# Optimization experiments

Measured on AMD Instinct MI355X. Metric: run time of the kernel, lower is better.

## Reference

```python
import jax, jax.numpy as jnp
import numpy as np

EPS = 1e-6


def _ring_view(t, start, length, M):
    # contiguous logical view of `length` oldest positions starting at start
    if start + length <= M:
        return t[:, start:start + length]
    first = t[:, start:]
    return jnp.concatenate([first, t[:, :length - first.shape[1]]], axis=1)


def _ring_write(t, start, chunk, M):
    # write chunk at logical position `start`, wrapping around the ring
    C = chunk.shape[1]
    if start + C <= M:
        return t.at[:, start:start + C].set(chunk)
    first = M - start
    t = t.at[:, start:].set(chunk[:, :first])
    return t.at[:, :C - first].set(chunk[:, first:])


def setup_inputs() -> dict:
    key = jax.random.key(0)
    ks = jax.random.split(key, 9)
    B, M, Hh, D, F, C = 4, 1088, 32, 128, 128, 512
    f = lambda k, s: jax.random.normal(k, s, dtype=jnp.float32)
    return {
        "K": f(ks[0], (B, M, Hh, D)),
        "V": f(ks[1], (B, M, Hh, D)),
        "FK": f(ks[2], (B, M, Hh, F)),
        "H": f(ks[3], (B, Hh, F, D)),
        "S": f(ks[4], (B, Hh, F)),
        "k_c": f(ks[5], (B, C, Hh, D)),
        "v_c": f(ks[6], (B, C, Hh, D)),
        "fk_c": f(ks[7], (B, C, Hh, F)),
        "fq": f(ks[8], (B, C, Hh, F)),
        "write_ptr": 100,
        "valid": 1088,
    }


def reference(K, V, FK, H, S, k_c, v_c, fk_c, fq, write_ptr, valid):
    M = K.shape[1]
    C = k_c.shape[1]
    if valid + C <= M:
        # room left in ring buffer: plain write, no eviction
        pos = (write_ptr + valid) % M
        K = _ring_write(K, pos, k_c, M)
        V = _ring_write(V, pos, v_c, M)
        FK = _ring_write(FK, pos, fk_c, M)
    else:
        # evict num_excess oldest tokens into recurrent state H, S
        num_excess = valid + C - M
        old_fk = _ring_view(FK, write_ptr, num_excess, M)  # (B, E, H, F)
        old_v = _ring_view(V, write_ptr, num_excess, M)    # (B, E, H, D)
        H = H + jnp.einsum('behf,behd->bhfd', old_fk, old_v)
        S = S + old_fk.sum(axis=1)
        write_ptr = (write_ptr + num_excess) % M
        pos = (write_ptr + M) % M  # valid == M now
        K = _ring_write(K, pos, k_c, M)
        V = _ring_write(V, pos, v_c, M)
        FK = _ring_write(FK, pos, fk_c, M)
    # linear_attn_forward(fq)
    y_num = jnp.einsum('bchf,bhfd->bchd', fq, H)
    y_den = jnp.einsum('bchf,bhf->bch', fq, S)[..., None]
    return y_num, y_den, K, V, FK, H, S
```

## Files before the change

kernel.cpp:

```cpp
#include <hip/hip_runtime.h>

constexpr int B  = 4;
constexpr int M  = 1088;
constexpr int HH = 32;
constexpr int D  = 128;
constexpr int F  = 128;
constexpr int C  = 512;

constexpr int SZ_YNUM = B * C * HH * D;
constexpr int SZ_YDEN = B * C * HH;
constexpr int SZ_KVM  = B * M * HH * D;
constexpr int SZ_H    = B * HH * F * D;

constexpr int OFF_YNUM = 0;
constexpr int OFF_YDEN = OFF_YNUM + SZ_YNUM;
constexpr int OFF_K    = OFF_YDEN + SZ_YDEN;
constexpr int OFF_V    = OFF_K + SZ_KVM;
constexpr int OFF_FK   = OFF_V + SZ_KVM;
constexpr int OFF_H    = OFF_FK + SZ_KVM;
constexpr int OFF_S    = OFF_H + SZ_H;

constexpr int INNER4      = HH * D / 4;
constexpr int ROWS_PER_CB = 4;
constexpr int COPY_BLOCKS = B * M / ROWS_PER_CB;
constexpr int HS_BLOCKS   = B * HH * 2;
constexpr int Y_BLOCKS    = B * HH * 8;

__device__ __forceinline__ void ring_params(const int* wp_p, const int* valid_p,
                                            int& wp, int& num_excess, int& pos) {
    wp = *wp_p;
    int valid = *valid_p;
    if (valid + C <= M) {
        num_excess = 0;
        pos = (wp + valid) % M;
    } else {
        num_excess = valid + C - M;
        pos = (wp + num_excess) % M;
    }
}

__device__ __forceinline__ void ring_copy_block(int cb, int tid,
                                                const float4* __restrict__ src,
                                                const float4* __restrict__ chk,
                                                float4* __restrict__ dst,
                                                int pos) {
    int bm0 = cb * ROWS_PER_CB;
#pragma unroll
    for (int r = 0; r < ROWS_PER_CB; ++r) {
        int bm = bm0 + r;
        int m = bm % M;
        int b = bm / M;
        int off = m - pos;
        if (off < 0) off += M;
        const float4* s = (off < C) ? &chk[(b * C + off) * INNER4]
                                    : &src[bm * INNER4];
        float4* d = &dst[bm * INNER4];
#pragma unroll
        for (int k = 0; k < INNER4 / 256; ++k)
            d[k * 256 + tid] = s[k * 256 + tid];
    }
}

constexpr int ESTEP = 16;

__device__ void update_hs_body(int bx,
                               const float* __restrict__ FKi,
                               const float* __restrict__ Vi,
                               const float* __restrict__ Hi,
                               const float* __restrict__ Si,
                               float* __restrict__ Ho,
                               float* __restrict__ So,
                               int wp, int num_excess) {
    const int tid = threadIdx.x;
    const int fhalf = bx & 1;
    const int bh = bx >> 1;
    const int h = bh & (HH - 1);
    const int b = bh >> 5;
    const int fbase = fhalf * 64;

    __shared__ float  fk_s[ESTEP][64];
    __shared__ float4 v_s[ESTEP][32];
    __shared__ float  sred[4][64];

    const int tf = tid >> 5;
    const int td = tid & 31;
    const int cq = tid & 63;
    const int qq = tid >> 6;

    float acc[8][4];
#pragma unroll
    for (int i = 0; i < 8; ++i)
#pragma unroll
        for (int j = 0; j < 4; ++j) acc[i][j] = 0.f;
    float s_part = 0.f;

    float  fk_r[4];
    float4 v_r[2];

    auto load_tile = [&](int e0) {
#pragma unroll
        for (int j = 0; j < 4; ++j) {
            int e = e0 + qq + 4 * j;
            int me = wp + e;
            if (me >= M) me -= M;
            if (me >= M) me -= M;
            float v = 0.f;
            if (e < num_excess) v = FKi[((b * M + me) * HH + h) * F + fbase + cq];
            fk_r[j] = v;
        }
#pragma unroll
        for (int j = 0; j < 2; ++j) {
            int e = e0 + tf + 8 * j;
            int me = wp + e;
            if (me >= M) me -= M;
            if (me >= M) me -= M;
            float4 v = make_float4(0.f, 0.f, 0.f, 0.f);
            if (e < num_excess) v = *(const float4*)&Vi[((b * M + me) * HH + h) * D + td * 4];
            v_r[j] = v;
        }
    };
    auto store_tile = [&]() {
#pragma unroll
        for (int j = 0; j < 4; ++j) fk_s[qq + 4 * j][cq] = fk_r[j];
#pragma unroll
        for (int j = 0; j < 2; ++j) v_s[tf + 8 * j][td] = v_r[j];
    };

    if (num_excess > 0) {
        load_tile(0);
        store_tile();
        for (int e0 = 0; e0 < num_excess; e0 += ESTEP) {
            bool more = (e0 + ESTEP < num_excess);
            if (more) load_tile(e0 + ESTEP);
            __syncthreads();
#pragma unroll
            for (int ee = 0; ee < ESTEP; ++ee) {
                float4 vv = v_s[ee][td];
#pragma unroll
                for (int i = 0; i < 8; ++i) {
                    float f = fk_s[ee][tf * 8 + i];
                    acc[i][0] += f * vv.x; acc[i][1] += f * vv.y;
                    acc[i][2] += f * vv.z; acc[i][3] += f * vv.w;
                }
            }
#pragma unroll
            for (int j = 0; j < 4; ++j) s_part += fk_s[qq * 4 + j][cq];
            __syncthreads();
            if (more) store_tile();
        }
    }

    sred[qq][cq] = s_part;
    __syncthreads();
    if (tid < 64) {
        int f = fbase + tid;
        int si = (b * HH + h) * F + f;
        So[si] = Si[si] + sred[0][tid] + sred[1][tid] + sred[2][tid] + sred[3][tid];
    }

#pragma unroll
    for (int i = 0; i < 8; ++i) {
        int f = fbase + tf * 8 + i;
        int base = ((b * HH + h) * F + f) * D + td * 4;
        float4 hold = *(const float4*)&Hi[base];
        *(float4*)&Ho[base] = make_float4(hold.x + acc[i][0], hold.y + acc[i][1],
                                          hold.z + acc[i][2], hold.w + acc[i][3]);
    }
}

__device__ void compute_y_den_body(int bx,
                                   const float* __restrict__ fq,
                                   const float* __restrict__ Hn,
                                   const float* __restrict__ Sn,
                                   float* __restrict__ ynum,
                                   float* __restrict__ yden) {
    const int tid = threadIdx.x;
    int t = bx;
    const int ct = t & 7; t >>= 3;
    const int h = t & (HH - 1);
    const int b = t >> 5;
    const int c0 = ct * 64;

    __shared__ float  fq_s[32][65];
    __shared__ float4 h_s[32][32];
    __shared__ float  S_s[128];
    __shared__ float  den_s[64][4];

    const int tc = tid >> 5;
    const int td = tid & 31;
    const int cq = tid & 63;
    const int qq = tid >> 6;

    if (tid < 128) S_s[tid] = Sn[(b * HH + h) * F + tid];

    float acc[8][4];
#pragma unroll
    for (int i = 0; i < 8; ++i)
#pragma unroll
        for (int j = 0; j < 4; ++j) acc[i][j] = 0.f;
    float den_part = 0.f;

    for (int f0 = 0; f0 < F; f0 += 32) {
#pragma unroll
        for (int r = 0; r < 8; ++r) {
            int idx = tid + r * 256;
            int cc = idx >> 5, ee = idx & 31;
            fq_s[ee][cc] = fq[((b * C + c0 + cc) * HH + h) * F + f0 + ee];
        }
#pragma unroll
        for (int r = 0; r < 4; ++r) {
            int idx = tid + r * 256;
            int row = idx >> 5, col = idx & 31;
            h_s[row][col] = *(const float4*)&Hn[((b * HH + h) * F + f0 + row) * D + col * 4];
        }
        __syncthreads();
#pragma unroll
        for (int ee = 0; ee < 32; ++ee) {
            float4 hv = h_s[ee][td];
#pragma unroll
            for (int i = 0; i < 8; ++i) {
                float q = fq_s[ee][tc * 8 + i];
                acc[i][0] += q * hv.x; acc[i][1] += q * hv.y;
                acc[i][2] += q * hv.z; acc[i][3] += q * hv.w;
            }
        }
#pragma unroll
        for (int j = 0; j < 8; ++j)
            den_part += fq_s[qq * 8 + j][cq] * S_s[f0 + qq * 8 + j];
        __syncthreads();
    }

    den_s[cq][qq] = den_part;
    __syncthreads();
    if (tid < 64)
        yden[(b * C + c0 + tid) * HH + h] =
            den_s[tid][0] + den_s[tid][1] + den_s[tid][2] + den_s[tid][3];

#pragma unroll
    for (int i = 0; i < 8; ++i) {
        int c = c0 + tc * 8 + i;
        int base = ((b * C + c) * HH + h) * D + td * 4;
        *(float4*)&ynum[base] = make_float4(acc[i][0], acc[i][1], acc[i][2], acc[i][3]);
    }
}

__global__ __launch_bounds__(256) void fused_hs_vfk(
        const float* __restrict__ FKi, const float* __restrict__ Vi,
        const float* __restrict__ Hi,  const float* __restrict__ Si,
        float* __restrict__ Ho,        float* __restrict__ So,
        const float4* __restrict__ V4, const float4* __restrict__ vc, float4* __restrict__ oV,
        const float4* __restrict__ FK4,const float4* __restrict__ fkc,float4* __restrict__ oFK,
        const int* __restrict__ wp_p,  const int* __restrict__ valid_p) {
    int wp, num_excess, pos;
    ring_params(wp_p, valid_p, wp, num_excess, pos);

    int bx = blockIdx.x;
    if (bx < HS_BLOCKS) {
        update_hs_body(bx, FKi, Vi, Hi, Si, Ho, So, wp, num_excess);
        return;
    }
    bx -= HS_BLOCKS;
    if (bx < COPY_BLOCKS) {
        ring_copy_block(bx, threadIdx.x, V4, vc, oV, pos);
        return;
    }
    bx -= COPY_BLOCKS;
    ring_copy_block(bx, threadIdx.x, FK4, fkc, oFK, pos);
}

__global__ __launch_bounds__(256) void fused_y_k(
        const float* __restrict__ fq, const float* __restrict__ Hn,
        const float* __restrict__ Sn,
        float* __restrict__ ynum,     float* __restrict__ yden,
        const float4* __restrict__ K4, const float4* __restrict__ kc,
        float4* __restrict__ oK,
        const int* __restrict__ wp_p,  const int* __restrict__ valid_p) {
    int wp, num_excess, pos;
    ring_params(wp_p, valid_p, wp, num_excess, pos);

    int bx = blockIdx.x;
    if (bx < Y_BLOCKS) {
        compute_y_den_body(bx, fq, Hn, Sn, ynum, yden);
        return;
    }
    bx -= Y_BLOCKS;
    ring_copy_block(bx, threadIdx.x, K4, kc, oK, pos);
}

extern "C" void kernel_launch(void* const* d_in, const int* in_sizes, int n_in,
                              void* d_out, int out_size, void* d_ws, size_t ws_size,
                              hipStream_t stream) {
    const float* K   = (const float*)d_in[0];
    const float* V   = (const float*)d_in[1];
    const float* FK  = (const float*)d_in[2];
    const float* H   = (const float*)d_in[3];
    const float* S   = (const float*)d_in[4];
    const float* k_c = (const float*)d_in[5];
    const float* v_c = (const float*)d_in[6];
    const float* fk_c= (const float*)d_in[7];
    const float* fq  = (const float*)d_in[8];
    const int* wp    = (const int*)d_in[9];
    const int* valid = (const int*)d_in[10];

    float* out = (float*)d_out;
    float* o_ynum = out + OFF_YNUM;
    float* o_yden = out + OFF_YDEN;
    float* o_K    = out + OFF_K;
    float* o_V    = out + OFF_V;
    float* o_FK   = out + OFF_FK;
    float* o_H    = out + OFF_H;
    float* o_S    = out + OFF_S;

    fused_hs_vfk<<<HS_BLOCKS + 2 * COPY_BLOCKS, 256, 0, stream>>>(
        FK, V, H, S, o_H, o_S,
        (const float4*)V,  (const float4*)v_c,  (float4*)o_V,
        (const float4*)FK, (const float4*)fk_c, (float4*)o_FK,
        wp, valid);

    fused_y_k<<<Y_BLOCKS + COPY_BLOCKS, 256, 0, stream>>>(
        fq, o_H, o_S, o_ynum, o_yden,
        (const float4*)K, (const float4*)k_c, (float4*)o_K,
        wp, valid);
}
```

Measured before the change: 127.6 us.

## Move K ring copy into first kernel, use nontemporal copies, widen eviction tile

The K ring-buffer copy moves out of the y-computation kernel into the first kernel, so all three large ring copies run together and the second kernel only computes y_num and y_den. The ring copies, the H reads and the y_num stores now use nontemporal loads and stores, to keep streaming data from polluting the cache. The H/S eviction tile grows from 16 to 32 tokens, halving the number of tile iterations and barriers. The inner FMA loops use native 4-wide vector types with vectorized shared-memory reads of FK. Risks: a larger, copy-heavy first kernel, and possible slowdowns from the nontemporal hints or the larger shared-memory footprint.

```diff
diff --git a/kernel.cpp b/kernel.cpp
--- a/kernel.cpp
+++ b/kernel.cpp
@@ -1,4 +1,6 @@
 #include <hip/hip_runtime.h>
+
+typedef float f32x4 __attribute__((ext_vector_type(4)));
 
 constexpr int B  = 4;
 constexpr int M  = 1088;
@@ -40,9 +42,9 @@
 }
 
 __device__ __forceinline__ void ring_copy_block(int cb, int tid,
-                                                const float4* __restrict__ src,
-                                                const float4* __restrict__ chk,
-                                                float4* __restrict__ dst,
+                                                const f32x4* __restrict__ src,
+                                                const f32x4* __restrict__ chk,
+                                                f32x4* __restrict__ dst,
                                                 int pos) {
     int bm0 = cb * ROWS_PER_CB;
 #pragma unroll
@@ -52,16 +54,21 @@
         int b = bm / M;
         int off = m - pos;
         if (off < 0) off += M;
-        const float4* s = (off < C) ? &chk[(b * C + off) * INNER4]
-                                    : &src[bm * INNER4];
-        float4* d = &dst[bm * INNER4];
-#pragma unroll
-        for (int k = 0; k < INNER4 / 256; ++k)
-            d[k * 256 + tid] = s[k * 256 + tid];
-    }
-}
-
-constexpr int ESTEP = 16;
+        const f32x4* s = (off < C) ? &chk[(b * C + off) * INNER4]
+                                   : &src[bm * INNER4];
+        f32x4* d = &dst[bm * INNER4];
+        f32x4 t0 = __builtin_nontemporal_load(s + tid);
+        f32x4 t1 = __builtin_nontemporal_load(s + 256 + tid);
+        f32x4 t2 = __builtin_nontemporal_load(s + 512 + tid);
+        f32x4 t3 = __builtin_nontemporal_load(s + 768 + tid);
+        __builtin_nontemporal_store(t0, d + tid);
+        __builtin_nontemporal_store(t1, d + 256 + tid);
+        __builtin_nontemporal_store(t2, d + 512 + tid);
+        __builtin_nontemporal_store(t3, d + 768 + tid);
+    }
+}
+
+constexpr int ESTEP = 32;
 
 __device__ void update_hs_body(int bx,
                                const float* __restrict__ FKi,
@@ -79,7 +86,7 @@
     const int fbase = fhalf * 64;
 
     __shared__ float  fk_s[ESTEP][64];
-    __shared__ float4 v_s[ESTEP][32];
+    __shared__ f32x4  v_s[ESTEP][32];
     __shared__ float  sred[4][64];
 
     const int tf = tid >> 5;
@@ -87,19 +94,17 @@
     const int cq = tid & 63;
     const int qq = tid >> 6;
 
-    float acc[8][4];
-#pragma unroll
-    for (int i = 0; i < 8; ++i)
-#pragma unroll
-        for (int j = 0; j < 4; ++j) acc[i][j] = 0.f;
+    f32x4 acc[8];
+#pragma unroll
+    for (int i = 0; i < 8; ++i) acc[i] = (f32x4)0.f;
     float s_part = 0.f;
 
-    float  fk_r[4];
-    float4 v_r[2];
+    float fk_r[8];
+    f32x4 v_r[4];
 
     auto load_tile = [&](int e0) {
 #pragma unroll
-        for (int j = 0; j < 4; ++j) {
+        for (int j = 0; j < 8; ++j) {
             int e = e0 + qq + 4 * j;
             int me = wp + e;
             if (me >= M) me -= M;
@@ -109,21 +114,21 @@
             fk_r[j] = v;
         }
 #pragma unroll
-        for (int j = 0; j < 2; ++j) {
+        for (int j = 0; j < 4; ++j) {
             int e = e0 + tf + 8 * j;
             int me = wp + e;
             if (me >= M) me -= M;
             if (me >= M) me -= M;
-            float4 v = make_float4(0.f, 0.f, 0.f, 0.f);
-            if (e < num_excess) v = *(const float4*)&Vi[((b * M + me) * HH + h) * D + td * 4];
+            f32x4 v = (f32x4)0.f;
+            if (e < num_excess) v = *(const f32x4*)&Vi[((b * M + me) * HH + h) * D + td * 4];
             v_r[j] = v;
         }
     };
     auto store_tile = [&]() {
 #pragma unroll
-        for (int j = 0; j < 4; ++j) fk_s[qq + 4 * j][cq] = fk_r[j];
-#pragma unroll
-        for (int j = 0; j < 2; ++j) v_s[tf + 8 * j][td] = v_r[j];
+        for (int j = 0; j < 8; ++j) fk_s[qq + 4 * j][cq] = fk_r[j];
+#pragma unroll
+        for (int j = 0; j < 4; ++j) v_s[tf + 8 * j][td] = v_r[j];
     };
 
     if (num_excess > 0) {
@@ -135,16 +140,16 @@
             __syncthreads();
 #pragma unroll
             for (int ee = 0; ee < ESTEP; ++ee) {
-                float4 vv = v_s[ee][td];
-#pragma unroll
-                for (int i = 0; i < 8; ++i) {
-                    float f = fk_s[ee][tf * 8 + i];
-                    acc[i][0] += f * vv.x; acc[i][1] += f * vv.y;
-                    acc[i][2] += f * vv.z; acc[i][3] += f * vv.w;
-                }
+                f32x4 fa = *(const f32x4*)&fk_s[ee][tf * 8];
+                f32x4 fb = *(const f32x4*)&fk_s[ee][tf * 8 + 4];
+                f32x4 vv = v_s[ee][td];
+                acc[0] += fa.x * vv; acc[1] += fa.y * vv;
+                acc[2] += fa.z * vv; acc[3] += fa.w * vv;
+                acc[4] += fb.x * vv; acc[5] += fb.y * vv;
+                acc[6] += fb.z * vv; acc[7] += fb.w * vv;
             }
 #pragma unroll
-            for (int j = 0; j < 4; ++j) s_part += fk_s[qq * 4 + j][cq];
+            for (int j = 0; j < 8; ++j) s_part += fk_s[qq * 8 + j][cq];
             __syncthreads();
             if (more) store_tile();
         }
@@ -162,9 +167,8 @@
     for (int i = 0; i < 8; ++i) {
         int f = fbase + tf * 8 + i;
         int base = ((b * HH + h) * F + f) * D + td * 4;
-        float4 hold = *(const float4*)&Hi[base];
-        *(float4*)&Ho[base] = make_float4(hold.x + acc[i][0], hold.y + acc[i][1],
-                                          hold.z + acc[i][2], hold.w + acc[i][3]);
+        f32x4 hold = __builtin_nontemporal_load((const f32x4*)&Hi[base]);
+        *(f32x4*)&Ho[base] = hold + acc[i];
     }
 }
 
@@ -182,7 +186,7 @@
     const int c0 = ct * 64;
 
     __shared__ float  fq_s[32][65];
-    __shared__ float4 h_s[32][32];
+    __shared__ f32x4  h_s[32][32];
     __shared__ float  S_s[128];
     __shared__ float  den_s[64][4];
 
@@ -193,11 +197,9 @@
 
     if (tid < 128) S_s[tid] = Sn[(b * HH + h) * F + tid];
 
-    float acc[8][4];
-#pragma unroll
-    for (int i = 0; i < 8; ++i)
-#pragma unroll
-        for (int j = 0; j < 4; ++j) acc[i][j] = 0.f;
+    f32x4 acc[8];
+#pragma unroll
+    for (int i = 0; i < 8; ++i) acc[i] = (f32x4)0.f;
     float den_part = 0.f;
 
     for (int f0 = 0; f0 < F; f0 += 32) {
@@ -205,23 +207,23 @@
         for (int r = 0; r < 8; ++r) {
             int idx = tid + r * 256;
             int cc = idx >> 5, ee = idx & 31;
-            fq_s[ee][cc] = fq[((b * C + c0 + cc) * HH + h) * F + f0 + ee];
+            fq_s[ee][cc] = __builtin_nontemporal_load(
+                &fq[((b * C + c0 + cc) * HH + h) * F + f0 + ee]);
         }
 #pragma unroll
         for (int r = 0; r < 4; ++r) {
             int idx = tid + r * 256;
             int row = idx >> 5, col = idx & 31;
-            h_s[row][col] = *(const float4*)&Hn[((b * HH + h) * F + f0 + row) * D + col * 4];
+            h_s[row][col] = *(const f32x4*)&Hn[((b * HH + h) * F + f0 + row) * D + col * 4];
         }
         __syncthreads();
 #pragma unroll
         for (int ee = 0; ee < 32; ++ee) {
-            float4 hv = h_s[ee][td];
+            f32x4 hv = h_s[ee][td];
 #pragma unroll
             for (int i = 0; i < 8; ++i) {
                 float q = fq_s[ee][tc * 8 + i];
-                acc[i][0] += q * hv.x; acc[i][1] += q * hv.y;
-                acc[i][2] += q * hv.z; acc[i][3] += q * hv.w;
+                acc[i] += q * hv;
             }
         }
 #pragma unroll
@@ -240,16 +242,17 @@
     for (int i = 0; i < 8; ++i) {
         int c = c0 + tc * 8 + i;
         int base = ((b * C + c) * HH + h) * D + td * 4;
-        *(float4*)&ynum[base] = make_float4(acc[i][0], acc[i][1], acc[i][2], acc[i][3]);
-    }
-}
-
-__global__ __launch_bounds__(256) void fused_hs_vfk(
+        __builtin_nontemporal_store(acc[i], (f32x4*)&ynum[base]);
+    }
+}
+
+__global__ __launch_bounds__(256) void fused_hs_copy(
         const float* __restrict__ FKi, const float* __restrict__ Vi,
         const float* __restrict__ Hi,  const float* __restrict__ Si,
         float* __restrict__ Ho,        float* __restrict__ So,
-        const float4* __restrict__ V4, const float4* __restrict__ vc, float4* __restrict__ oV,
-        const float4* __restrict__ FK4,const float4* __restrict__ fkc,float4* __restrict__ oFK,
+        const f32x4* __restrict__ V4,  const f32x4* __restrict__ vc,  f32x4* __restrict__ oV,
+        const f32x4* __restrict__ FK4, const f32x4* __restrict__ fkc, f32x4* __restrict__ oFK,
+        const f32x4* __restrict__ K4,  const f32x4* __restrict__ kc,  f32x4* __restrict__ oK,
         const int* __restrict__ wp_p,  const int* __restrict__ valid_p) {
     int wp, num_excess, pos;
     ring_params(wp_p, valid_p, wp, num_excess, pos);
@@ -265,26 +268,19 @@
         return;
     }
     bx -= COPY_BLOCKS;
-    ring_copy_block(bx, threadIdx.x, FK4, fkc, oFK, pos);
-}
-
-__global__ __launch_bounds__(256) void fused_y_k(
+    if (bx < COPY_BLOCKS) {
+        ring_copy_block(bx, threadIdx.x, FK4, fkc, oFK, pos);
+        return;
+    }
+    bx -= COPY_BLOCKS;
+    ring_copy_block(bx, threadIdx.x, K4, kc, oK, pos);
+}
+
+__global__ __launch_bounds__(256) void fused_y(
         const float* __restrict__ fq, const float* __restrict__ Hn,
         const float* __restrict__ Sn,
-        float* __restrict__ ynum,     float* __restrict__ yden,
-        const float4* __restrict__ K4, const float4* __restrict__ kc,
-        float4* __restrict__ oK,
-        const int* __restrict__ wp_p,  const int* __restrict__ valid_p) {
-    int wp, num_excess, pos;
-    ring_params(wp_p, valid_p, wp, num_excess, pos);
-
-    int bx = blockIdx.x;
-    if (bx < Y_BLOCKS) {
-        compute_y_den_body(bx, fq, Hn, Sn, ynum, yden);
-        return;
-    }
-    bx -= Y_BLOCKS;
-    ring_copy_block(bx, threadIdx.x, K4, kc, oK, pos);
+        float* __restrict__ ynum,     float* __restrict__ yden) {
+    compute_y_den_body(blockIdx.x, fq, Hn, Sn, ynum, yden);
 }
 
 extern "C" void kernel_launch(void* const* d_in, const int* in_sizes, int n_in,
@@ -311,14 +307,12 @@
     float* o_H    = out + OFF_H;
     float* o_S    = out + OFF_S;
 
-    fused_hs_vfk<<<HS_BLOCKS + 2 * COPY_BLOCKS, 256, 0, stream>>>(
+    fused_hs_copy<<<HS_BLOCKS + 3 * COPY_BLOCKS, 256, 0, stream>>>(
         FK, V, H, S, o_H, o_S,
-        (const float4*)V,  (const float4*)v_c,  (float4*)o_V,
-        (const float4*)FK, (const float4*)fk_c, (float4*)o_FK,
+        (const f32x4*)V,  (const f32x4*)v_c,  (f32x4*)o_V,
+        (const f32x4*)FK, (const f32x4*)fk_c, (f32x4*)o_FK,
+        (const f32x4*)K,  (const f32x4*)k_c,  (f32x4*)o_K,
         wp, valid);
 
-    fused_y_k<<<Y_BLOCKS + COPY_BLOCKS, 256, 0, stream>>>(
-        fq, o_H, o_S, o_ynum, o_yden,
-        (const float4*)K, (const float4*)k_c, (float4*)o_K,
-        wp, valid);
-}
+    fused_y<<<Y_BLOCKS, 256, 0, stream>>>(fq, o_H, o_S, o_ynum, o_yden);
+}
```

Result: slower. 139.7 us (+9.5%).
